# Kernel tuning notes

Hardware: AMD Instinct MI355X
Metric: run time of the kernel (lower is better)

## Reference

```python
import jax, jax.numpy as jnp
import numpy as np

B, D, T = 32, 1024, 1000
LMAX = 200
VOCAB = 80
BLANK = VOCAB - 1
NEG = -1e30


def setup_inputs() -> dict:
    key = jax.random.key(0)
    ks = jax.random.split(key, 8)
    decoder_outputs = jax.random.normal(ks[0], (B, D, T), dtype=jnp.float32)
    target_text = jax.random.randint(ks[1], (B, LMAX), 0, BLANK, dtype=jnp.int32)
    decoder_lengths = jax.random.randint(ks[2], (B,), T // 2, T + 1, dtype=jnp.int32)
    target_lengths = jax.random.randint(ks[3], (B,), 1, LMAX + 1, dtype=jnp.int32)
    # learned params (dropout is identity in eval / deterministic reference)
    W1 = jax.random.normal(ks[4], (D, D), dtype=jnp.float32) * (1.0 / np.sqrt(D))
    b1 = jnp.zeros((D,), dtype=jnp.float32)
    W2 = jax.random.normal(ks[5], (D, VOCAB), dtype=jnp.float32) * (1.0 / np.sqrt(D))
    b2 = jnp.zeros((VOCAB,), dtype=jnp.float32)
    return {"decoder_outputs": decoder_outputs, "target_text": target_text,
            "decoder_lengths": decoder_lengths, "target_lengths": target_lengths,
            "W1": W1, "b1": b1, "W2": W2, "b2": b2}


def _ctc_nll(log_probs, targets, input_lengths, target_lengths):
    # log_probs: [T, B, V]; standard CTC alpha (forward) DP over extended labels.
    Tt, Bb, V = log_probs.shape
    L = targets.shape[1]
    S = 2 * L + 1
    ext = jnp.full((Bb, S), BLANK, dtype=targets.dtype).at[:, 1::2].set(targets)
    ext_m2 = jnp.pad(ext, ((0, 0), (2, 0)), constant_values=BLANK)[:, :S]
    allow_skip = (ext != BLANK) & (ext != ext_m2)
    allow_skip = allow_skip.at[:, :2].set(False)

    lp0 = log_probs[0]  # [B, V]
    alpha0 = jnp.full((Bb, S), NEG, dtype=log_probs.dtype)
    alpha0 = alpha0.at[:, 0].set(lp0[:, BLANK])
    alpha0 = alpha0.at[:, 1].set(jnp.take_along_axis(lp0, targets[:, :1], axis=1)[:, 0])

    def step(alpha, inp):
        lp_t, t = inp
        emit = jnp.take_along_axis(lp_t, ext, axis=1)  # [B, S]
        a2 = jnp.pad(alpha, ((0, 0), (1, 0)), constant_values=NEG)[:, :S]
        a3 = jnp.pad(alpha, ((0, 0), (2, 0)), constant_values=NEG)[:, :S]
        a3 = jnp.where(allow_skip, a3, NEG)
        new = jnp.logaddexp(jnp.logaddexp(alpha, a2), a3) + emit
        alpha = jnp.where((t < input_lengths)[:, None], new, alpha)
        return alpha, None

    alpha, _ = jax.lax.scan(step, alpha0, (log_probs[1:], jnp.arange(1, Tt)))
    i1 = (2 * target_lengths - 1)[:, None]
    i2 = (2 * target_lengths)[:, None]
    last = jnp.logaddexp(jnp.take_along_axis(alpha, i1, axis=1)[:, 0],
                         jnp.take_along_axis(alpha, i2, axis=1)[:, 0])
    nll = -last
    # zero_infinity=True: invalid alignments -> 0 loss
    return jnp.where(last > NEG / 2, nll, 0.0)


def reference(decoder_outputs, target_text, decoder_lengths, target_lengths, W1, b1, W2, b2):
    x = jnp.transpose(decoder_outputs, (0, 2, 1))          # [B, T, D]
    h = jax.nn.relu(jnp.einsum('btd,de->bte', x, W1) + b1)  # proj + ReLU (dropout=identity)
    logits = jnp.einsum('btd,dv->btv', h, W2) + b2          # [B, T, V]
    log_probs = jax.nn.log_softmax(logits, axis=2)
    log_probs = jnp.transpose(log_probs, (1, 0, 2))         # [T, B, V]
    ctc_loss = _ctc_nll(log_probs, target_text, decoder_lengths, target_lengths)
    return (ctc_loss / decoder_lengths.astype(jnp.float32)).mean()
```

## Files before the change

### kernel.cpp

```cpp
#include <hip/hip_runtime.h>
#include <cstdint>
#include <cstddef>

#define BN_ 32
#define DD_ 1024
#define TT_ 1000
#define LMAX_ 200
#define VC_ 80
#define BLANK_ 79
#define SS_ 401
#define SPAD 512
#define NEGV (-1e30f)

typedef _Float16 half8 __attribute__((ext_vector_type(8)));
typedef float f32x4 __attribute__((ext_vector_type(4)));

__device__ __forceinline__ void async16(const void* g, void* l) {
  __builtin_amdgcn_global_load_lds(
      (const __attribute__((address_space(1))) unsigned int*)g,
      (__attribute__((address_space(3))) unsigned int*)l, 16, 0, 0);
}

__global__ __launch_bounds__(256) void transpose_all_kernel(
    const float* __restrict__ dec, const float* __restrict__ W1,
    const float* __restrict__ W2, _Float16* __restrict__ Af,
    _Float16* __restrict__ W1T, _Float16* __restrict__ W2T) {
  __shared__ _Float16 T[64][72];
  int z = blockIdx.z;
  const float* in; _Float16* out; int C;
  const int R = 1024;
  if (z < 32) {
    in = dec + (size_t)z * R * TT_;
    out = Af + (size_t)z * TT_ * R;
    C = TT_;
  } else if (z == 32) {
    in = W1; out = W1T; C = 1024;
  } else {
    in = W2; out = W2T; C = VC_;
  }
  int c0 = blockIdx.x * 64, r0 = blockIdx.y * 64;
  if (c0 >= C) return;
  int tid = threadIdx.x;
  int cl = tid & 63, rg = tid >> 6;
  int c = c0 + cl;
  bool cv = (c < C);
  const float* ip = in + (size_t)(r0 + rg * 16) * C + c;
  _Float16 h[16];
#pragma unroll
  for (int i = 0; i < 16; ++i) h[i] = cv ? (_Float16)ip[(size_t)i * C] : (_Float16)0.f;
  *(half8*)&T[cl][rg * 16] = *(half8*)&h[0];
  *(half8*)&T[cl][rg * 16 + 8] = *(half8*)&h[8];
  __syncthreads();
  int cr = tid >> 2, rc = (tid & 3) * 16;
  if (c0 + cr < C) {
    half8 a = *(const half8*)&T[cr][rc];
    half8 b2 = *(const half8*)&T[cr][rc + 8];
    _Float16* op = out + (size_t)(c0 + cr) * R + r0 + rc;
    *(half8*)op = a;
    *(half8*)(op + 8) = b2;
  }
}

__global__ __launch_bounds__(256) void gemm_relu_kernel(
    const _Float16* __restrict__ A, const _Float16* __restrict__ Bt,
    const float* __restrict__ bias, _Float16* __restrict__ H,
    int M, int N, int K) {
  constexpr int BK = 64;
  __shared__ __align__(16) _Float16 sA[128 * BK];
  __shared__ __align__(16) _Float16 sB[128 * BK];
  int tid = threadIdx.x;
  int wave = tid >> 6, lane = tid & 63;
  int quad = lane >> 4, r16 = lane & 15;
  int m0 = blockIdx.y * 128, n0 = blockIdx.x * 128;
  int moff = (wave >> 1) * 64, noff = (wave & 1) * 64;

  f32x4 acc[4][4];
#pragma unroll
  for (int i = 0; i < 4; ++i)
#pragma unroll
    for (int j = 0; j < 4; ++j) acc[i][j] = {0.f, 0.f, 0.f, 0.f};

  for (int kt = 0; kt < K; kt += BK) {
#pragma unroll
    for (int jj = 0; jj < 4; ++jj) {
      int seg = tid + 256 * jj;
      int row = seg >> 3, slot = seg & 7;
      int cg = slot ^ (row & 7);
      async16(A + (size_t)(m0 + row) * K + kt + cg * 8, &sA[seg * 8]);
      async16(Bt + (size_t)(n0 + row) * K + kt + cg * 8, &sB[seg * 8]);
    }
    __syncthreads();
#pragma unroll
    for (int ku = 0; ku < 2; ++ku) {
      int sw = ((ku * 4 + quad) ^ (r16 & 7)) * 8;
      half8 af[4], bfr[4];
#pragma unroll
      for (int i = 0; i < 4; ++i)
        af[i] = *(const half8*)&sA[(moff + i * 16 + r16) * BK + sw];
#pragma unroll
      for (int j = 0; j < 4; ++j)
        bfr[j] = *(const half8*)&sB[(noff + j * 16 + r16) * BK + sw];
#pragma unroll
      for (int i = 0; i < 4; ++i)
#pragma unroll
        for (int j = 0; j < 4; ++j)
          acc[i][j] = __builtin_amdgcn_mfma_f32_16x16x32_f16(af[i], bfr[j], acc[i][j], 0, 0, 0);
    }
    __syncthreads();
  }
#pragma unroll
  for (int j = 0; j < 4; ++j) {
    int n = n0 + noff + j * 16 + r16;
    float bv = bias[n];
#pragma unroll
    for (int i = 0; i < 4; ++i) {
#pragma unroll
      for (int r = 0; r < 4; ++r) {
        int m = m0 + moff + i * 16 + quad * 4 + r;
        float v = acc[i][j][r] + bv;
        v = fmaxf(v, 0.f);
        H[(size_t)m * N + n] = (_Float16)v;
      }
    }
  }
}

__global__ __launch_bounds__(256) void gemm_prob_kernel(
    const _Float16* __restrict__ A, const _Float16* __restrict__ Bt,
    const float* __restrict__ bias, float* __restrict__ P, int M, int K) {
  constexpr int BK = 64;
  __shared__ __align__(16) _Float16 sA[64 * BK];
  __shared__ __align__(16) _Float16 sB[VC_ * BK];
  int tid = threadIdx.x;
  int wave = tid >> 6, lane = tid & 63;
  int quad = lane >> 4, r16 = lane & 15;
  int m0 = blockIdx.x * 64;

  f32x4 acc[5];
#pragma unroll
  for (int j = 0; j < 5; ++j) acc[j] = {0.f, 0.f, 0.f, 0.f};

  for (int kt = 0; kt < K; kt += BK) {
#pragma unroll
    for (int jj = 0; jj < 2; ++jj) {
      int seg = tid + 256 * jj;
      int row = seg >> 3, slot = seg & 7;
      int cg = slot ^ (row & 7);
      async16(A + (size_t)(m0 + row) * K + kt + cg * 8, &sA[seg * 8]);
    }
#pragma unroll
    for (int jj = 0; jj < 3; ++jj) {
      int seg = tid + 256 * jj;
      if (seg < VC_ * 8) {
        int row = seg >> 3, slot = seg & 7;
        int cg = slot ^ (row & 7);
        async16(Bt + (size_t)row * K + kt + cg * 8, &sB[seg * 8]);
      }
    }
    __syncthreads();
#pragma unroll
    for (int ku = 0; ku < 2; ++ku) {
      int sw = ((ku * 4 + quad) ^ (r16 & 7)) * 8;
      half8 af = *(const half8*)&sA[(wave * 16 + r16) * BK + sw];
      half8 bfr[5];
#pragma unroll
      for (int j = 0; j < 5; ++j)
        bfr[j] = *(const half8*)&sB[(j * 16 + r16) * BK + sw];
#pragma unroll
      for (int j = 0; j < 5; ++j)
        acc[j] = __builtin_amdgcn_mfma_f32_16x16x32_f16(af, bfr[j], acc[j], 0, 0, 0);
    }
    __syncthreads();
  }
  float bv[5];
#pragma unroll
  for (int j = 0; j < 5; ++j) bv[j] = bias[j * 16 + r16];
#pragma unroll
  for (int rr = 0; rr < 4; ++rr) {
    float vals[5];
    float mx = -3.4e38f;
#pragma unroll
    for (int j = 0; j < 5; ++j) {
      vals[j] = acc[j][rr] + bv[j];
      mx = fmaxf(mx, vals[j]);
    }
#pragma unroll
    for (int d = 1; d < 16; d <<= 1) mx = fmaxf(mx, __shfl_xor(mx, d));
    float ex[5], sm = 0.f;
#pragma unroll
    for (int j = 0; j < 5; ++j) { ex[j] = __expf(vals[j] - mx); sm += ex[j]; }
#pragma unroll
    for (int d = 1; d < 16; d <<= 1) sm += __shfl_xor(sm, d);
    float rinv = 1.f / sm;
    int m = m0 + wave * 16 + quad * 4 + rr;
    float* o = P + (size_t)m * VC_;
#pragma unroll
    for (int j = 0; j < 5; ++j) o[j * 16 + r16] = ex[j] * rinv;
  }
}

__global__ __launch_bounds__(256) void emit_kernel(
    const float* __restrict__ P, const int* __restrict__ targets,
    float* __restrict__ EM) {
  int idx = blockIdx.x * 256 + threadIdx.x;
  int s = idx & (SPAD - 1);
  int bt = idx >> 9;
  float v = 0.f;
  if (s < SS_) {
    int lab = BLANK_;
    if (s & 1) {
      int b = bt / TT_;
      lab = targets[b * LMAX_ + (s >> 1)];
    }
    v = P[(size_t)bt * VC_ + lab];
  }
  EM[idx] = v;
}

__device__ __forceinline__ void dp_step_fwd(float (&bta)[8], int& k,
                                            const f32x4 e0, const f32x4 e1,
                                            const float (&am)[4], int lane) {
  float pm1 = __shfl_up(bta[7], 1);
  int pk = __shfl_up(k, 1);
  if (lane == 0) { pm1 = 0.f; pk = k; }
  int knew = max(k, pk);
  pm1 = ldexpf(pm1, pk - knew);
  int ds = k - knew;
#pragma unroll
  for (int r = 0; r < 8; ++r) bta[r] = ldexpf(bta[r], ds);
  k = knew;
  float nb[8];
  nb[0] = (bta[0] + pm1) * e0.x;
  nb[1] = fmaf(am[0], pm1, bta[1] + bta[0]) * e0.y;
  nb[2] = (bta[2] + bta[1]) * e0.z;
  nb[3] = fmaf(am[1], bta[1], bta[3] + bta[2]) * e0.w;
  nb[4] = (bta[4] + bta[3]) * e1.x;
  nb[5] = fmaf(am[2], bta[3], bta[5] + bta[4]) * e1.y;
  nb[6] = (bta[6] + bta[5]) * e1.z;
  nb[7] = fmaf(am[3], bta[5], bta[7] + bta[6]) * e1.w;
#pragma unroll
  for (int r = 0; r < 8; ++r) bta[r] = nb[r];
}

__device__ __forceinline__ void dp_step_bwd(float (&g)[8], int& k,
                                            const f32x4 e0, const f32x4 e1,
                                            const float (&amB)[4], int lane) {
  float gh[8];
  gh[0] = g[0] * e0.x; gh[1] = g[1] * e0.y;
  gh[2] = g[2] * e0.z; gh[3] = g[3] * e0.w;
  gh[4] = g[4] * e1.x; gh[5] = g[5] * e1.y;
  gh[6] = g[6] * e1.z; gh[7] = g[7] * e1.w;
  float qm1 = __shfl_down(gh[0], 1);
  float qm2 = __shfl_down(gh[1], 1);
  int nk = __shfl_down(k, 1);
  if (lane == 63) { qm1 = 0.f; qm2 = 0.f; nk = k; }
  int knew = max(k, nk);
  int dq = nk - knew;
  qm1 = ldexpf(qm1, dq);
  qm2 = ldexpf(qm2, dq);
  int ds = k - knew;
#pragma unroll
  for (int r = 0; r < 8; ++r) gh[r] = ldexpf(gh[r], ds);
  k = knew;
  g[0] = gh[0] + gh[1];
  g[1] = fmaf(amB[0], gh[3], gh[1] + gh[2]);
  g[2] = gh[2] + gh[3];
  g[3] = fmaf(amB[1], gh[5], gh[3] + gh[4]);
  g[4] = gh[4] + gh[5];
  g[5] = fmaf(amB[2], gh[7], gh[5] + gh[6]);
  g[6] = gh[6] + gh[7];
  g[7] = fmaf(amB[3], qm2, gh[7] + qm1);
}

__device__ __forceinline__ void dp_rescale(float (&v)[8], int& k) {
  float m = fmaxf(fmaxf(fmaxf(v[0], v[1]), fmaxf(v[2], v[3])),
                  fmaxf(fmaxf(v[4], v[5]), fmaxf(v[6], v[7])));
  int ex = (__float_as_int(m) >> 23) - 126;
  k += ex;
#pragma unroll
  for (int r = 0; r < 8; ++r) v[r] = ldexpf(v[r], -ex);
}

__device__ __forceinline__ float allow_f(const int* __restrict__ tg, int s) {
  if (!(s & 1) || s < 3) return 0.f;
  int li = s >> 1;
  if (li >= LMAX_) return 0.f;
  int lab = tg[li];
  return (lab != BLANK_ && lab != tg[li - 1]) ? 1.f : 0.f;
}

__global__ __launch_bounds__(128) void ctc_dp_kernel(
    const float* __restrict__ EM, const int* __restrict__ targets,
    const int* __restrict__ dlen, const int* __restrict__ tlen,
    float* __restrict__ out) {
  __shared__ float sg[SPAD];
  __shared__ int skg[64];
  int b = blockIdx.x;
  int wave = threadIdx.x >> 6;
  int lane = threadIdx.x & 63;
  const float* em = EM + (size_t)b * TT_ * SPAD + lane * 8;
  const int* tg = targets + b * LMAX_;
  int Tl = dlen[b], Ll = tlen[b];
  int tm = Tl >> 1;

  constexpr int PD = 8;
  f32x4 pf[PD][2];
  float v[8];
  int k = 0;

  if (wave == 0) {
    float am[4];
#pragma unroll
    for (int j = 0; j < 4; ++j) am[j] = allow_f(tg, lane * 8 + 2 * j + 1);
    f32x4 r0a = *(const f32x4*)(em);
#pragma unroll
    for (int r = 0; r < 8; ++r) v[r] = 0.f;
    if (lane == 0) { v[0] = r0a.x; v[1] = r0a.y; }
#pragma unroll
    for (int j = 0; j < PD; ++j) {
      int ri = min(1 + j, TT_ - 1);
      pf[j][0] = *(const f32x4*)(em + (size_t)ri * SPAD);
      pf[j][1] = *(const f32x4*)(em + (size_t)ri * SPAD + 4);
    }
    int t = 1;
    for (; t + (PD - 1) <= tm; t += PD) {
#pragma unroll
      for (int u = 0; u < PD; ++u) {
        dp_step_fwd(v, k, pf[u][0], pf[u][1], am, lane);
        if (u & 1) dp_rescale(v, k);
        int ri = min(t + u + PD, TT_ - 1);
        pf[u][0] = *(const f32x4*)(em + (size_t)ri * SPAD);
        pf[u][1] = *(const f32x4*)(em + (size_t)ri * SPAD + 4);
      }
    }
#pragma unroll
    for (int u = 0; u < PD; ++u) {
      if (t + u <= tm) {
        dp_step_fwd(v, k, pf[u][0], pf[u][1], am, lane);
        if (u & 1) dp_rescale(v, k);
      }
    }
  } else {
    float amB[4];
#pragma unroll
    for (int j = 0; j < 4; ++j) amB[j] = allow_f(tg, lane * 8 + 2 * j + 3);
    int s1 = 2 * Ll - 1, s2 = 2 * Ll;
#pragma unroll
    for (int r = 0; r < 8; ++r) {
      int s = lane * 8 + r;
      v[r] = (s == s1 || s == s2) ? 1.f : 0.f;
    }
#pragma unroll
    for (int j = 0; j < PD; ++j) {
      int ri = max(Tl - 1 - j, 0);
      pf[j][0] = *(const f32x4*)(em + (size_t)ri * SPAD);
      pf[j][1] = *(const f32x4*)(em + (size_t)ri * SPAD + 4);
    }
    int t = Tl - 1;
    for (; t - (PD - 1) > tm; t -= PD) {
#pragma unroll
      for (int u = 0; u < PD; ++u) {
        dp_step_bwd(v, k, pf[u][0], pf[u][1], amB, lane);
        if (u & 1) dp_rescale(v, k);
        int ri = max(t - u - PD, 0);
        pf[u][0] = *(const f32x4*)(em + (size_t)ri * SPAD);
        pf[u][1] = *(const f32x4*)(em + (size_t)ri * SPAD + 4);
      }
    }
#pragma unroll
    for (int u = 0; u < PD; ++u) {
      if (t - u > tm) {
        dp_step_bwd(v, k, pf[u][0], pf[u][1], amB, lane);
        if (u & 1) dp_rescale(v, k);
      }
    }
#pragma unroll
    for (int r = 0; r < 8; ++r) sg[lane * 8 + r] = v[r];
    skg[lane] = k;
  }
  __syncthreads();
  if (wave == 0) {
    float p = 0.f;
#pragma unroll
    for (int r = 0; r < 8; ++r) p = fmaf(v[r], sg[lane * 8 + r], p);
    int kk = k + skg[lane];
    if (p == 0.f) kk = -(1 << 30);
#pragma unroll
    for (int d = 1; d < 64; d <<= 1) {
      float po = __shfl_xor(p, d);
      int ko = __shfl_xor(kk, d);
      int km = max(kk, ko);
      p = ldexpf(p, kk - km) + ldexpf(po, ko - km);
      kk = km;
    }
    if (lane == 0) {
      float nll = 0.f;
      if (p > 0.f) nll = -((log2f(p) + (float)kk) * 0.69314718055994531f);
      atomicAdd(out, nll / (float)Tl * (1.f / BN_));
    }
  }
}

extern "C" void kernel_launch(void* const* d_in, const int* in_sizes, int n_in,
                              void* d_out, int out_size, void* d_ws, size_t ws_size,
                              hipStream_t stream) {
  const float* dec = (const float*)d_in[0];
  const int* tgt   = (const int*)d_in[1];
  const int* dln   = (const int*)d_in[2];
  const int* tln   = (const int*)d_in[3];
  const float* W1  = (const float*)d_in[4];
  const float* b1  = (const float*)d_in[5];
  const float* W2  = (const float*)d_in[6];
  const float* b2  = (const float*)d_in[7];
  float* out = (float*)d_out;

  char* ws = (char*)d_ws;
  const size_t M = (size_t)BN_ * TT_;
  _Float16* Af   = (_Float16*)(ws);
  float* EM      = (float*)(ws);
  _Float16* Hf   = (_Float16*)(ws + 65536000);
  _Float16* W1T  = (_Float16*)(ws + 131072000);
  _Float16* W2T  = (_Float16*)(ws + 133169152);
  float* Pp      = (float*)(ws + 133332992);

  hipMemsetAsync(d_out, 0, sizeof(float), stream);

  transpose_all_kernel<<<dim3(16, 16, 34), 256, 0, stream>>>(
      dec, W1, W2, Af, W1T, W2T);
  gemm_relu_kernel<<<dim3(DD_ / 128, M / 128, 1), 256, 0, stream>>>(
      Af, W1T, b1, Hf, (int)M, DD_, DD_);
  gemm_prob_kernel<<<dim3(M / 64, 1, 1), 256, 0, stream>>>(
      Hf, W2T, b2, Pp, (int)M, DD_);
  emit_kernel<<<dim3((BN_ * TT_ * SPAD) / 256, 1, 1), 256, 0, stream>>>(Pp, tgt, EM);
  ctc_dp_kernel<<<dim3(BN_, 1, 1), 128, 0, stream>>>(EM, tgt, dln, tln, out);
}
```

Measured before the change: 438.6 us.

## Rewrite first GEMM with 256x256 tiles, double-buffered LDS pipeline and XCD remap

The 1024x1024 projection GEMM moves from 128x128 tiles with 256 threads and a synchronous load/compute loop to 256x256 tiles with 512 threads. Global-to-LDS loads are split into half tiles and issued between MFMA phases across two LDS buffers, with explicit vmcnt waits, barriers and setprio. A block-index remap groups tiles by XCD so neighbouring tiles share L2. The aim is to hide load latency and raise MFMA utilisation. In exchange it uses much more LDS and registers per block, which can lower occupancy. The hand-written wait counts are fragile.

Result: faster. 418.6 us (-4.6%).

```diff
diff --git a/kernel.cpp b/kernel.cpp
--- a/kernel.cpp
+++ b/kernel.cpp
@@ -61,67 +61,122 @@
   }
 }
 
-__global__ __launch_bounds__(256) void gemm_relu_kernel(
+__device__ __forceinline__ void stage_half(const _Float16* __restrict__ X,
+                                           int x0, int kt, int h,
+                                           _Float16* lds, int tid, int K) {
+#pragma unroll
+  for (int jj = 0; jj < 2; ++jj) {
+    int seg = tid + 512 * jj;
+    int row = seg >> 3, slot = seg & 7;
+    int cg = slot ^ (row & 7);
+    async16(X + (size_t)(x0 + h * 128 + row) * K + kt * 64 + cg * 8,
+            lds + seg * 8);
+  }
+}
+
+__global__ __launch_bounds__(512, 2) void gemm_relu_kernel(
     const _Float16* __restrict__ A, const _Float16* __restrict__ Bt,
     const float* __restrict__ bias, _Float16* __restrict__ H,
     int M, int N, int K) {
-  constexpr int BK = 64;
-  __shared__ __align__(16) _Float16 sA[128 * BK];
-  __shared__ __align__(16) _Float16 sB[128 * BK];
+  __shared__ __align__(16) _Float16 sA[2][16384];
+  __shared__ __align__(16) _Float16 sB[2][16384];
   int tid = threadIdx.x;
   int wave = tid >> 6, lane = tid & 63;
   int quad = lane >> 4, r16 = lane & 15;
-  int m0 = blockIdx.y * 128, n0 = blockIdx.x * 128;
-  int moff = (wave >> 1) * 64, noff = (wave & 1) * 64;
-
-  f32x4 acc[4][4];
-#pragma unroll
-  for (int i = 0; i < 4; ++i)
-#pragma unroll
-    for (int j = 0; j < 4; ++j) acc[i][j] = {0.f, 0.f, 0.f, 0.f};
-
-  for (int kt = 0; kt < K; kt += BK) {
-#pragma unroll
-    for (int jj = 0; jj < 4; ++jj) {
-      int seg = tid + 256 * jj;
-      int row = seg >> 3, slot = seg & 7;
-      int cg = slot ^ (row & 7);
-      async16(A + (size_t)(m0 + row) * K + kt + cg * 8, &sA[seg * 8]);
-      async16(Bt + (size_t)(n0 + row) * K + kt + cg * 8, &sB[seg * 8]);
-    }
-    __syncthreads();
-#pragma unroll
-    for (int ku = 0; ku < 2; ++ku) {
-      int sw = ((ku * 4 + quad) ^ (r16 & 7)) * 8;
-      half8 af[4], bfr[4];
+  int wm = wave >> 2, wn = wave & 3;
+
+  int orig = blockIdx.x, nwg = gridDim.x;
+  int xcd = orig & 7, loc = orig >> 3;
+  int qq = nwg >> 3, rr = nwg & 7;
+  int wg = (xcd < rr ? xcd * (qq + 1) : rr * (qq + 1) + (xcd - rr) * qq) + loc;
+  int m0 = (wg >> 2) * 256, n0 = (wg & 3) * 256;
+
+  f32x4 acc[4][8];
+#pragma unroll
+  for (int q = 0; q < 4; ++q)
+#pragma unroll
+    for (int f = 0; f < 8; ++f) acc[q][f] = {0.f, 0.f, 0.f, 0.f};
+
+  stage_half(A, m0, 0, 0, &sA[0][0], tid, K);
+  stage_half(A, m0, 0, 1, &sA[0][8192], tid, K);
+  stage_half(Bt, n0, 0, 0, &sB[0][0], tid, K);
+  stage_half(Bt, n0, 0, 1, &sB[0][8192], tid, K);
+  stage_half(A, m0, 1, 0, &sA[1][0], tid, K);
+  stage_half(Bt, n0, 1, 0, &sB[1][0], tid, K);
+  stage_half(A, m0, 1, 1, &sA[1][8192], tid, K);
+  asm volatile("s_waitcnt vmcnt(6)" ::: "memory");
+  __builtin_amdgcn_s_barrier();
+
+  const int NKT = K >> 6;
+#pragma unroll 2
+  for (int t = 0; t < NKT; ++t) {
+    int cur = t & 1, nxt = cur ^ 1;
+    int t1 = (t + 1 < NKT) ? t + 1 : NKT - 1;
+    int t2 = (t + 2 < NKT) ? t + 2 : NKT - 1;
+    const _Float16* As = sA[cur];
+    const _Float16* Bs = sB[cur];
+#pragma unroll
+    for (int q = 0; q < 4; ++q) {
+      const int qm = q >> 1, qn = q & 1;
+      half8 af[4][2], bf[2][2];
+      int abase = (qm * 128 + wm * 64 + r16) * 64;
+      int bbase = (qn * 128 + wn * 32 + r16) * 64;
+      int sw0 = ((0 * 4 + quad) ^ (r16 & 7)) * 8;
+      int sw1 = ((1 * 4 + quad) ^ (r16 & 7)) * 8;
+#pragma unroll
+      for (int i = 0; i < 4; ++i) {
+        af[i][0] = *(const half8*)&As[abase + i * 16 * 64 + sw0];
+        af[i][1] = *(const half8*)&As[abase + i * 16 * 64 + sw1];
+      }
+#pragma unroll
+      for (int j = 0; j < 2; ++j) {
+        bf[j][0] = *(const half8*)&Bs[bbase + j * 16 * 64 + sw0];
+        bf[j][1] = *(const half8*)&Bs[bbase + j * 16 * 64 + sw1];
+      }
+      if (q == 0) stage_half(Bt, n0, t1, 1, &sB[nxt][8192], tid, K);
+      else if (q == 1) stage_half(A, m0, t2, 0, &sA[cur][0], tid, K);
+      else if (q == 2) stage_half(Bt, n0, t2, 0, &sB[cur][0], tid, K);
+      else stage_half(A, m0, t2, 1, &sA[cur][8192], tid, K);
+      __builtin_amdgcn_s_barrier();
+      asm volatile("s_waitcnt lgkmcnt(0)" ::: "memory");
+      __builtin_amdgcn_s_setprio(1);
 #pragma unroll
       for (int i = 0; i < 4; ++i)
-        af[i] = *(const half8*)&sA[(moff + i * 16 + r16) * BK + sw];
-#pragma unroll
-      for (int j = 0; j < 4; ++j)
-        bfr[j] = *(const half8*)&sB[(noff + j * 16 + r16) * BK + sw];
-#pragma unroll
-      for (int i = 0; i < 4; ++i)
-#pragma unroll
-        for (int j = 0; j < 4; ++j)
-          acc[i][j] = __builtin_amdgcn_mfma_f32_16x16x32_f16(af[i], bfr[j], acc[i][j], 0, 0, 0);
-    }
-    __syncthreads();
-  }
-#pragma unroll
-  for (int j = 0; j < 4; ++j) {
-    int n = n0 + noff + j * 16 + r16;
-    float bv = bias[n];
-#pragma unroll
-    for (int i = 0; i < 4; ++i) {
-#pragma unroll
-      for (int r = 0; r < 4; ++r) {
-        int m = m0 + moff + i * 16 + quad * 4 + r;
-        float v = acc[i][j][r] + bv;
-        v = fmaxf(v, 0.f);
-        H[(size_t)m * N + n] = (_Float16)v;
-      }
-    }
+#pragma unroll
+        for (int j = 0; j < 2; ++j) {
+          acc[q][i * 2 + j] = __builtin_amdgcn_mfma_f32_16x16x32_f16(
+              af[i][0], bf[j][0], acc[q][i * 2 + j], 0, 0, 0);
+          acc[q][i * 2 + j] = __builtin_amdgcn_mfma_f32_16x16x32_f16(
+              af[i][1], bf[j][1], acc[q][i * 2 + j], 0, 0, 0);
+        }
+      __builtin_amdgcn_s_setprio(0);
+      if (q == 3) asm volatile("s_waitcnt vmcnt(6)" ::: "memory");
+      __builtin_amdgcn_s_barrier();
+    }
+  }
+  asm volatile("s_waitcnt vmcnt(0)" ::: "memory");
+
+  float bvv[2][2];
+#pragma unroll
+  for (int qn = 0; qn < 2; ++qn)
+#pragma unroll
+    for (int j = 0; j < 2; ++j)
+      bvv[qn][j] = bias[n0 + qn * 128 + wn * 32 + j * 16 + r16];
+#pragma unroll
+  for (int q = 0; q < 4; ++q) {
+    const int qm = q >> 1, qn = q & 1;
+#pragma unroll
+    for (int i = 0; i < 4; ++i)
+#pragma unroll
+      for (int j = 0; j < 2; ++j) {
+#pragma unroll
+        for (int r = 0; r < 4; ++r) {
+          int m = m0 + qm * 128 + wm * 64 + i * 16 + quad * 4 + r;
+          int n = n0 + qn * 128 + wn * 32 + j * 16 + r16;
+          float v = acc[q][i * 2 + j][r] + bvv[qn][j];
+          H[(size_t)m * N + n] = (_Float16)fmaxf(v, 0.f);
+        }
+      }
   }
 }
 
@@ -427,7 +482,7 @@
 
   transpose_all_kernel<<<dim3(16, 16, 34), 256, 0, stream>>>(
       dec, W1, W2, Af, W1T, W2T);
-  gemm_relu_kernel<<<dim3(DD_ / 128, M / 128, 1), 256, 0, stream>>>(
+  gemm_relu_kernel<<<dim3((1024 / 256) * (M / 256), 1, 1), 512, 0, stream>>>(
       Af, W1T, b1, Hf, (int)M, DD_, DD_);
   gemm_prob_kernel<<<dim3(M / 64, 1, 1), 256, 0, stream>>>(
       Hf, W2T, b2, Pp, (int)M, DD_);
```
